# Performance work log

Hardware: AMD Instinct MI355X
Metric: run time of the kernel (lower is better)

## Reference

```python
import jax, jax.numpy as jnp
import numpy as np

B, C, T_TEXT, T_FEAT = 16, 256, 512, 4096
DELTA = 0.1  # temperature


def setup_inputs() -> dict:
    key = jax.random.key(0)
    k1, k2 = jax.random.split(key)
    x = jax.random.normal(k1, (B, C, T_TEXT), dtype=jnp.float32)
    # durations: avg ~8 frames per token so cumsum spans ~T_FEAT frames
    w = jax.random.uniform(k2, (B, T_TEXT), dtype=jnp.float32) * 16.0
    x_mask = jnp.ones((B, T_FEAT), dtype=bool)   # frame-level mask (B, T_feat)
    y_mask = jnp.ones((B, T_TEXT), dtype=bool)   # token-level mask (B, T_text)
    return {"x": x, "w": w, "x_mask": x_mask, "y_mask": y_mask}


def reference(x, w, x_mask, y_mask):
    # x: (B, C, T_text), w: (B, T_text)
    t_feat = x_mask.shape[-1]
    # frame time grid, masked frames zeroed as in reference impl
    t = jnp.arange(t_feat, dtype=x.dtype)[None, :] * x_mask.astype(x.dtype)  # (B, T_feat)
    # Gaussian centers per token: cumulative duration minus half of own duration
    c = jnp.cumsum(w, axis=-1) - 0.5 * w  # (B, T_text)
    # energy: -delta * (t - c)^2  -> (B, T_feat, T_text)
    energy = -DELTA * jnp.square(t[:, :, None] - c[:, None, :])
    energy = jnp.where(y_mask[:, None, :], energy, -jnp.inf)
    attn = jax.nn.softmax(energy, axis=-1)  # softmax over tokens (T_text)
    # weighted sum over tokens: (B, T_feat, T_text) x (B, C, T_text) -> (B, C, T_feat)
    return jnp.einsum('bft,bct->bcf', attn, x)
```

## Files before the change

### kernel.cpp

```cpp
#include <hip/hip_runtime.h>
#include <math.h>


constexpr int BB  = 16;
constexpr int CC  = 256;
constexpr int TT  = 512;
constexpr int TF  = 4096;
constexpr float DEL = 0.1f;

constexpr int TILE_F = 32;
constexpr int MAXW   = 32;
constexpr int MAXN   = 64;
constexpr float CUT  = 200.0f;

__global__ __launch_bounds__(64)
void centers_k(const float* __restrict__ w, float* __restrict__ cw) {
  const int b = blockIdx.x, l = threadIdx.x;
  const float* wr = w + b * TT + l * 8;
  float v[8];
  *(float4*)&v[0] = *(const float4*)&wr[0];
  *(float4*)&v[4] = *(const float4*)&wr[4];
  double s[8]; double run = 0.0;
#pragma unroll
  for (int k = 0; k < 8; ++k) { run += (double)v[k]; s[k] = run; }
  double tot = run;
  for (int off = 1; off < 64; off <<= 1) {
    double o = __shfl_up(tot, off, 64);
    if (l >= off) tot += o;
  }
  const double base = tot - run;
  float* co = cw + b * TT + l * 8;
#pragma unroll
  for (int k = 0; k < 8; ++k) co[k] = (float)(base + s[k] - 0.5 * (double)v[k]);
}

__global__ __launch_bounds__(256, 4)
void gauss_up(const float* __restrict__ x, const float* __restrict__ cw,
              float* __restrict__ out) {
  __shared__ float sc[TT];
  __shared__ __align__(16) float pbuf[MAXN][TILE_F];
  __shared__ int s_info[2];

  const int lin   = blockIdx.x;
  const int xcd   = lin & 7;
  const int slot  = lin >> 3;
  const int b     = xcd * 2 + (slot >> 7);
  const int ftile = slot & 127;
  const int f0    = ftile * TILE_F;
  const int tid   = threadIdx.x;

  sc[tid]       = cw[b * TT + tid];
  sc[tid + 256] = cw[b * TT + tid + 256];
#pragma unroll
  for (int k = 0; k < MAXN * TILE_F / 256; ++k)
    ((float*)pbuf)[tid + 256 * k] = 0.f;
  __syncthreads();

  if (tid < TILE_F) {
    const float fv = (float)(f0 + tid);
    int l = 0, h = TT;
    while (l < h) { int m = (l + h) >> 1; if (sc[m] < fv) l = m + 1; else h = m; }
    int jstar = (l < TT) ? l : TT - 1;
    float dmin = fabsf(sc[jstar] - fv);
    if (l > 0) { float d = fabsf(sc[l - 1] - fv); if (d <= dmin) { dmin = d; jstar = l - 1; } }
    const float D = sqrtf(fmaf(dmin, dmin, CUT));
    int lo = 0; h = TT;
    { const float lv = fv - D;
      while (lo < h) { int m = (lo + h) >> 1; if (sc[m] < lv) lo = m + 1; else h = m; } }
    int hi = lo; h = TT;
    { const float hv = fv + D;
      while (hi < h) { int m = (hi + h) >> 1; if (sc[m] <= hv) hi = m + 1; else h = m; } }
    if (hi - lo > MAXW) {
      int nl = jstar - MAXW / 2; if (nl < lo) nl = lo;
      lo = nl;
      if (hi > lo + MAXW) hi = lo + MAXW;
    }

    int LO = lo, HI = hi;
#pragma unroll
    for (int m = 16; m >= 1; m >>= 1) {
      LO = min(LO, __shfl_xor(LO, m, 32));
      HI = max(HI, __shfl_xor(HI, m, 32));
    }
    int LO4 = LO & ~3;
    if (HI - LO4 > MAXN) {
      const int js0  = __shfl(jstar, 0, 32);
      const int js31 = __shfl(jstar, 31, 32);
      int nl = (((js0 + js31) >> 1) - MAXN / 2) & ~3;
      if (nl < LO4) nl = LO4;
      LO4 = nl;
      if (HI > LO4 + MAXN) HI = LO4 + MAXN;
      if (lo < LO4) lo = LO4;
      if (hi > HI)  hi = HI;
      if (lo >= hi) {
        lo = min(max(jstar, LO4), HI - 1); hi = lo + 1;
      }
    }

    const int n_f = hi - lo;
    const int j0  = lo - LO4;
    const float m0 = DEL * dmin * dmin;
    float Z = 0.f;
    for (int j = 0; j < n_f; ++j) {
      const float d = fv - sc[lo + j];
      const float e = __expf(fmaf(-DEL, d * d, m0));
      pbuf[j0 + j][tid] = e;
      Z += e;
    }
    const float rz = 1.f / Z;
    for (int j = 0; j < n_f; ++j) pbuf[j0 + j][tid] *= rz;
    if (tid == 0) { s_info[0] = LO4; s_info[1] = (HI - LO4 + 3) >> 2; }
  }
  __syncthreads();

  const int LO4 = s_info[0];
  const int NC  = s_info[1];
  const int cg  = tid >> 2;
  const int fg  = tid & 3;

  const float* xr0 = x + ((size_t)b * CC + (size_t)cg * 4) * TT + LO4;

  float acc[4][8];
#pragma unroll
  for (int i = 0; i < 4; ++i)
#pragma unroll
    for (int k = 0; k < 8; ++k) acc[i][k] = 0.f;

  for (int jc = 0; jc < NC; ++jc) {
    float4 xv[4];
#pragma unroll
    for (int i = 0; i < 4; ++i)
      xv[i] = *(const float4*)(xr0 + (size_t)i * TT + 4 * jc);
#pragma unroll
    for (int jj = 0; jj < 4; ++jj) {
      const float4 p0 = *(const float4*)&pbuf[4 * jc + jj][fg * 8];
      const float4 p1 = *(const float4*)&pbuf[4 * jc + jj][fg * 8 + 4];
#pragma unroll
      for (int i = 0; i < 4; ++i) {
        const float xs = ((const float*)&xv[i])[jj];
        acc[i][0] = fmaf(p0.x, xs, acc[i][0]);
        acc[i][1] = fmaf(p0.y, xs, acc[i][1]);
        acc[i][2] = fmaf(p0.z, xs, acc[i][2]);
        acc[i][3] = fmaf(p0.w, xs, acc[i][3]);
        acc[i][4] = fmaf(p1.x, xs, acc[i][4]);
        acc[i][5] = fmaf(p1.y, xs, acc[i][5]);
        acc[i][6] = fmaf(p1.z, xs, acc[i][6]);
        acc[i][7] = fmaf(p1.w, xs, acc[i][7]);
      }
    }
  }

  float* orow = out + ((size_t)b * CC + (size_t)cg * 4) * TF + f0 + fg * 8;
#pragma unroll
  for (int i = 0; i < 4; ++i) {
    *(float4*)(orow + (size_t)i * TF)     =
        make_float4(acc[i][0], acc[i][1], acc[i][2], acc[i][3]);
    *(float4*)(orow + (size_t)i * TF + 4) =
        make_float4(acc[i][4], acc[i][5], acc[i][6], acc[i][7]);
  }
}

extern "C" void kernel_launch(void* const* d_in, const int* in_sizes, int n_in,
                              void* d_out, int out_size, void* d_ws, size_t ws_size,
                              hipStream_t stream) {
  const float* x = (const float*)d_in[0];
  const float* w = (const float*)d_in[1];
  float* out = (float*)d_out;
  float* cw  = (float*)d_ws;

  centers_k<<<dim3(BB), dim3(64), 0, stream>>>(w, cw);
  gauss_up<<<dim3(TF / TILE_F * BB), dim3(256), 0, stream>>>(x, cw, out);
}
```

Baseline: 96.13 us.

## Precompute attention windows in separate kernel and stream weights through workspace

Splits the work differently: a new per-tile kernel recomputes the cumsum centers, does the binary-search window and softmax weights, and writes the weight tile plus window info to workspace. The main kernel then only loads the precomputed weights and does the FMA accumulation, with nontemporal output stores. The goal is to take the serial 32-thread search/softmax phase, which idles most of the block, off the main kernel's critical path. The cost is about 8MB of extra workspace traffic and redundant cumsum work in every tile. A fallback path runs when the workspace is too small.

```diff
diff --git a/kernel.cpp b/kernel.cpp
--- a/kernel.cpp
+++ b/kernel.cpp
@@ -12,6 +12,175 @@
 constexpr int MAXW   = 32;
 constexpr int MAXN   = 64;
 constexpr float CUT  = 200.0f;
+
+constexpr int NTILE = TF / TILE_F * BB;
+constexpr int PBSZ  = MAXN * TILE_F;
+constexpr size_t WS_NEED = 16384 + (size_t)NTILE * PBSZ * 4;
+
+typedef float f32x4 __attribute__((ext_vector_type(4)));
+
+__device__ __forceinline__ void tile_map(int lin, int& b, int& f0) {
+  const int xcd  = lin & 7;
+  const int slot = lin >> 3;
+  b  = xcd * 2 + (slot >> 7);
+  f0 = (slot & 127) * TILE_F;
+}
+
+__global__ __launch_bounds__(64)
+void wins_k(const float* __restrict__ w, float* __restrict__ pb,
+            int2* __restrict__ info) {
+  __shared__ float sc[TT];
+  __shared__ __align__(16) float pbuf[MAXN][TILE_F];
+
+  int b, f0; tile_map(blockIdx.x, b, f0);
+  const int l = threadIdx.x;
+
+  const float* wr = w + b * TT + l * 8;
+  float v[8];
+  *(float4*)&v[0] = *(const float4*)&wr[0];
+  *(float4*)&v[4] = *(const float4*)&wr[4];
+  double s[8]; double run = 0.0;
+#pragma unroll
+  for (int k = 0; k < 8; ++k) { run += (double)v[k]; s[k] = run; }
+  double tot = run;
+  for (int off = 1; off < 64; off <<= 1) {
+    double o = __shfl_up(tot, off, 64);
+    if (l >= off) tot += o;
+  }
+  const double base = tot - run;
+#pragma unroll
+  for (int k = 0; k < 8; ++k)
+    sc[l * 8 + k] = (float)(base + s[k] - 0.5 * (double)v[k]);
+
+#pragma unroll
+  for (int k = 0; k < 8; ++k)
+    ((float4*)pbuf)[l + 64 * k] = make_float4(0.f, 0.f, 0.f, 0.f);
+  __syncthreads();
+
+  if (l < TILE_F) {
+    const float fv = (float)(f0 + l);
+    int lb = 0, h = TT;
+    while (lb < h) { int m = (lb + h) >> 1; if (sc[m] < fv) lb = m + 1; else h = m; }
+    int jstar = (lb < TT) ? lb : TT - 1;
+    float dmin = fabsf(sc[jstar] - fv);
+    if (lb > 0) { float d = fabsf(sc[lb - 1] - fv); if (d <= dmin) { dmin = d; jstar = lb - 1; } }
+    const float D = sqrtf(fmaf(dmin, dmin, CUT));
+    int lo = 0; h = TT;
+    { const float lv = fv - D;
+      while (lo < h) { int m = (lo + h) >> 1; if (sc[m] < lv) lo = m + 1; else h = m; } }
+    int hi = lo; h = TT;
+    { const float hv = fv + D;
+      while (hi < h) { int m = (hi + h) >> 1; if (sc[m] <= hv) hi = m + 1; else h = m; } }
+    if (hi - lo > MAXW) {
+      int nl = jstar - MAXW / 2; if (nl < lo) nl = lo;
+      lo = nl;
+      if (hi > lo + MAXW) hi = lo + MAXW;
+    }
+
+    int LO = lo, HI = hi;
+#pragma unroll
+    for (int m = 16; m >= 1; m >>= 1) {
+      LO = min(LO, __shfl_xor(LO, m, 32));
+      HI = max(HI, __shfl_xor(HI, m, 32));
+    }
+    int LO4 = LO & ~3;
+    if (HI - LO4 > MAXN) {
+      const int js0  = __shfl(jstar, 0, 32);
+      const int js31 = __shfl(jstar, 31, 32);
+      int nl = (((js0 + js31) >> 1) - MAXN / 2) & ~3;
+      if (nl < LO4) nl = LO4;
+      LO4 = nl;
+      if (HI > LO4 + MAXN) HI = LO4 + MAXN;
+      if (lo < LO4) lo = LO4;
+      if (hi > HI)  hi = HI;
+      if (lo >= hi) {
+        lo = min(max(jstar, LO4), HI - 1); hi = lo + 1;
+      }
+    }
+
+    const int n_f = hi - lo;
+    const int j0  = lo - LO4;
+    const float m0 = DEL * dmin * dmin;
+    float Z = 0.f;
+    for (int j = 0; j < n_f; ++j) {
+      const float d = fv - sc[lo + j];
+      const float e = __expf(fmaf(-DEL, d * d, m0));
+      pbuf[j0 + j][l] = e;
+      Z += e;
+    }
+    const float rz = 1.f / Z;
+    for (int j = 0; j < n_f; ++j) pbuf[j0 + j][l] *= rz;
+    if (l == 0) info[blockIdx.x] = make_int2(LO4, (HI - LO4 + 3) >> 2);
+  }
+  __syncthreads();
+
+  float4* dst = (float4*)(pb + (size_t)blockIdx.x * PBSZ);
+#pragma unroll
+  for (int k = 0; k < 8; ++k)
+    dst[l + 64 * k] = ((const float4*)pbuf)[l + 64 * k];
+}
+
+__global__ __launch_bounds__(256, 4)
+void gup2(const float* __restrict__ x, const float* __restrict__ pb,
+          const int2* __restrict__ info, float* __restrict__ out) {
+  __shared__ __align__(16) float pbuf[MAXN][TILE_F];
+
+  int b, f0; tile_map(blockIdx.x, b, f0);
+  const int tid = threadIdx.x;
+  const int2 nfo = info[blockIdx.x];
+
+  const float4* src = (const float4*)(pb + (size_t)blockIdx.x * PBSZ);
+  ((float4*)pbuf)[tid]       = src[tid];
+  ((float4*)pbuf)[tid + 256] = src[tid + 256];
+  __syncthreads();
+
+  const int LO4 = nfo.x;
+  const int NC  = nfo.y;
+  const int cg  = tid >> 2;
+  const int fg  = tid & 3;
+
+  const float* xr0 = x + ((size_t)b * CC + (size_t)cg * 4) * TT + LO4;
+
+  float acc[4][8];
+#pragma unroll
+  for (int i = 0; i < 4; ++i)
+#pragma unroll
+    for (int k = 0; k < 8; ++k) acc[i][k] = 0.f;
+
+  for (int jc = 0; jc < NC; ++jc) {
+    float4 xv[4];
+#pragma unroll
+    for (int i = 0; i < 4; ++i)
+      xv[i] = *(const float4*)(xr0 + (size_t)i * TT + 4 * jc);
+#pragma unroll
+    for (int jj = 0; jj < 4; ++jj) {
+      const float4 p0 = *(const float4*)&pbuf[4 * jc + jj][fg * 8];
+      const float4 p1 = *(const float4*)&pbuf[4 * jc + jj][fg * 8 + 4];
+#pragma unroll
+      for (int i = 0; i < 4; ++i) {
+        const float xs = ((const float*)&xv[i])[jj];
+        acc[i][0] = fmaf(p0.x, xs, acc[i][0]);
+        acc[i][1] = fmaf(p0.y, xs, acc[i][1]);
+        acc[i][2] = fmaf(p0.z, xs, acc[i][2]);
+        acc[i][3] = fmaf(p0.w, xs, acc[i][3]);
+        acc[i][4] = fmaf(p1.x, xs, acc[i][4]);
+        acc[i][5] = fmaf(p1.y, xs, acc[i][5]);
+        acc[i][6] = fmaf(p1.z, xs, acc[i][6]);
+        acc[i][7] = fmaf(p1.w, xs, acc[i][7]);
+      }
+    }
+  }
+
+  float* orow = out + ((size_t)b * CC + (size_t)cg * 4) * TF + f0 + fg * 8;
+#pragma unroll
+  for (int i = 0; i < 4; ++i) {
+    f32x4 v0 = {acc[i][0], acc[i][1], acc[i][2], acc[i][3]};
+    f32x4 v1 = {acc[i][4], acc[i][5], acc[i][6], acc[i][7]};
+    __builtin_nontemporal_store(v0, (f32x4*)(orow + (size_t)i * TF));
+    __builtin_nontemporal_store(v1, (f32x4*)(orow + (size_t)i * TF + 4));
+  }
+}
+
 
 __global__ __launch_bounds__(64)
 void centers_k(const float* __restrict__ w, float* __restrict__ cw) {
@@ -166,8 +335,15 @@
   const float* x = (const float*)d_in[0];
   const float* w = (const float*)d_in[1];
   float* out = (float*)d_out;
-  float* cw  = (float*)d_ws;
-
-  centers_k<<<dim3(BB), dim3(64), 0, stream>>>(w, cw);
-  gauss_up<<<dim3(TF / TILE_F * BB), dim3(256), 0, stream>>>(x, cw, out);
-}
+
+  if (ws_size >= WS_NEED) {
+    int2*  info = (int2*)d_ws;
+    float* pb   = (float*)d_ws + 4096;
+    wins_k<<<dim3(NTILE), dim3(64),  0, stream>>>(w, pb, info);
+    gup2  <<<dim3(NTILE), dim3(256), 0, stream>>>(x, pb, info, out);
+  } else {
+    float* cw = (float*)d_ws;
+    centers_k<<<dim3(BB),    dim3(64),  0, stream>>>(w, cw);
+    gauss_up <<<dim3(NTILE), dim3(256), 0, stream>>>(x, cw, out);
+  }
+}
```

Result: slower. 115.8 us (+20.5%).

## Precompute per-frame token windows in prep kernel and defer softmax normalization

Applied to the files above, without the earlier changes.

The per-frame binary searches for the Gaussian window move out of the main kernel into a wider prep kernel, which writes (argmin, lo, hi) per frame to workspace. The main kernel no longer stages centers or zeroes pbuf in shared memory. It computes exponentials over the whole tile window with vectorized center loads and masking, and applies 1/Z at output time. The thread mapping changes to 8 channels by 4 frames per thread. Using the union window per frame instead of each frame's own window changes numerics slightly and adds a workspace round trip.

```diff
diff --git a/kernel.cpp b/kernel.cpp
--- a/kernel.cpp
+++ b/kernel.cpp
@@ -13,70 +13,90 @@
 constexpr int MAXN   = 64;
 constexpr float CUT  = 200.0f;
 
-__global__ __launch_bounds__(64)
-void centers_k(const float* __restrict__ w, float* __restrict__ cw) {
-  const int b = blockIdx.x, l = threadIdx.x;
-  const float* wr = w + b * TT + l * 8;
-  float v[8];
-  *(float4*)&v[0] = *(const float4*)&wr[0];
-  *(float4*)&v[4] = *(const float4*)&wr[4];
-  double s[8]; double run = 0.0;
+constexpr int NTILE = TF / TILE_F * BB;
+constexpr size_t WS_CW  = (size_t)BB * TT * 4;
+constexpr size_t WS_NEED = WS_CW + (size_t)BB * TF * 8;
+
+__device__ __forceinline__ void tile_map(int lin, int& b, int& f0) {
+  const int xcd  = lin & 7;
+  const int slot = lin >> 3;
+  b  = xcd * 2 + (slot >> 7);
+  f0 = (slot & 127) * TILE_F;
+}
+
+__global__ __launch_bounds__(256)
+void prep_k(const float* __restrict__ w, float* __restrict__ cw,
+            ushort4* __restrict__ win) {
+  __shared__ float sc[TT];
+  const int b = blockIdx.x, tid = threadIdx.x;
+
+  if (tid < 64) {
+    const int l = tid;
+    const float* wr = w + b * TT + l * 8;
+    float v[8];
+    *(float4*)&v[0] = *(const float4*)&wr[0];
+    *(float4*)&v[4] = *(const float4*)&wr[4];
+    double s[8]; double run = 0.0;
 #pragma unroll
-  for (int k = 0; k < 8; ++k) { run += (double)v[k]; s[k] = run; }
-  double tot = run;
-  for (int off = 1; off < 64; off <<= 1) {
-    double o = __shfl_up(tot, off, 64);
-    if (l >= off) tot += o;
+    for (int k = 0; k < 8; ++k) { run += (double)v[k]; s[k] = run; }
+    double tot = run;
+    for (int off = 1; off < 64; off <<= 1) {
+      double o = __shfl_up(tot, off, 64);
+      if (l >= off) tot += o;
+    }
+    const double base = tot - run;
+    float c8[8];
+#pragma unroll
+    for (int k = 0; k < 8; ++k) c8[k] = (float)(base + s[k] - 0.5 * (double)v[k]);
+#pragma unroll
+    for (int k = 0; k < 8; ++k) sc[l * 8 + k] = c8[k];
+    if (blockIdx.y == 0) {
+      float* co = cw + b * TT + l * 8;
+#pragma unroll
+      for (int k = 0; k < 8; ++k) co[k] = c8[k];
+    }
   }
-  const double base = tot - run;
-  float* co = cw + b * TT + l * 8;
-#pragma unroll
-  for (int k = 0; k < 8; ++k) co[k] = (float)(base + s[k] - 0.5 * (double)v[k]);
+  __syncthreads();
+
+  const int f = blockIdx.y * 256 + tid;
+  const float fv = (float)f;
+  int lb = 0, h = TT;
+  while (lb < h) { int m = (lb + h) >> 1; if (sc[m] < fv) lb = m + 1; else h = m; }
+  int js = (lb < TT) ? lb : TT - 1;
+  float dmin = fabsf(sc[js] - fv);
+  if (lb > 0) { float d = fabsf(sc[lb - 1] - fv); if (d <= dmin) { dmin = d; js = lb - 1; } }
+  const float D = sqrtf(fmaf(dmin, dmin, CUT));
+  int lo = 0; h = TT;
+  { const float lv = fv - D;
+    while (lo < h) { int m = (lo + h) >> 1; if (sc[m] < lv) lo = m + 1; else h = m; } }
+  int hi = lo; h = TT;
+  { const float hv = fv + D;
+    while (hi < h) { int m = (hi + h) >> 1; if (sc[m] <= hv) hi = m + 1; else h = m; } }
+  if (hi - lo > MAXW) {
+    int nl = js - MAXW / 2; if (nl < lo) nl = lo;
+    lo = nl;
+    if (hi > lo + MAXW) hi = lo + MAXW;
+  }
+  win[b * TF + f] = make_ushort4((unsigned short)js, (unsigned short)lo,
+                                 (unsigned short)hi, 0);
 }
 
 __global__ __launch_bounds__(256, 4)
 void gauss_up(const float* __restrict__ x, const float* __restrict__ cw,
-              float* __restrict__ out) {
-  __shared__ float sc[TT];
+              const ushort4* __restrict__ win, float* __restrict__ out) {
   __shared__ __align__(16) float pbuf[MAXN][TILE_F];
+  __shared__ float srz[TILE_F];
   __shared__ int s_info[2];
 
-  const int lin   = blockIdx.x;
-  const int xcd   = lin & 7;
-  const int slot  = lin >> 3;
-  const int b     = xcd * 2 + (slot >> 7);
-  const int ftile = slot & 127;
-  const int f0    = ftile * TILE_F;
-  const int tid   = threadIdx.x;
-
-  sc[tid]       = cw[b * TT + tid];
-  sc[tid + 256] = cw[b * TT + tid + 256];
-#pragma unroll
-  for (int k = 0; k < MAXN * TILE_F / 256; ++k)
-    ((float*)pbuf)[tid + 256 * k] = 0.f;
-  __syncthreads();
+  int b, f0; tile_map(blockIdx.x, b, f0);
+  const int tid = threadIdx.x;
+  const float* cwb = cw + b * TT;
 
   if (tid < TILE_F) {
+    const ushort4 wv = win[b * TF + f0 + tid];
+    const int js = wv.x;
+    int LO = wv.y, HI = wv.z;
     const float fv = (float)(f0 + tid);
-    int l = 0, h = TT;
-    while (l < h) { int m = (l + h) >> 1; if (sc[m] < fv) l = m + 1; else h = m; }
-    int jstar = (l < TT) ? l : TT - 1;
-    float dmin = fabsf(sc[jstar] - fv);
-    if (l > 0) { float d = fabsf(sc[l - 1] - fv); if (d <= dmin) { dmin = d; jstar = l - 1; } }
-    const float D = sqrtf(fmaf(dmin, dmin, CUT));
-    int lo = 0; h = TT;
-    { const float lv = fv - D;
-      while (lo < h) { int m = (lo + h) >> 1; if (sc[m] < lv) lo = m + 1; else h = m; } }
-    int hi = lo; h = TT;
-    { const float hv = fv + D;
-      while (hi < h) { int m = (hi + h) >> 1; if (sc[m] <= hv) hi = m + 1; else h = m; } }
-    if (hi - lo > MAXW) {
-      int nl = jstar - MAXW / 2; if (nl < lo) nl = lo;
-      lo = nl;
-      if (hi > lo + MAXW) hi = lo + MAXW;
-    }
-
-    int LO = lo, HI = hi;
 #pragma unroll
     for (int m = 16; m >= 1; m >>= 1) {
       LO = min(LO, __shfl_xor(LO, m, 32));
@@ -84,79 +104,80 @@
     }
     int LO4 = LO & ~3;
     if (HI - LO4 > MAXN) {
-      const int js0  = __shfl(jstar, 0, 32);
-      const int js31 = __shfl(jstar, 31, 32);
+      const int js0  = __shfl(js, 0, 32);
+      const int js31 = __shfl(js, 31, 32);
       int nl = (((js0 + js31) >> 1) - MAXN / 2) & ~3;
       if (nl < LO4) nl = LO4;
       LO4 = nl;
       if (HI > LO4 + MAXN) HI = LO4 + MAXN;
-      if (lo < LO4) lo = LO4;
-      if (hi > HI)  hi = HI;
-      if (lo >= hi) {
-        lo = min(max(jstar, LO4), HI - 1); hi = lo + 1;
-      }
     }
-
-    const int n_f = hi - lo;
-    const int j0  = lo - LO4;
+    const int n  = HI - LO4;
+    const int NC = (n + 3) >> 2;
+    const float dmin = fabsf(fv - cwb[js]);
     const float m0 = DEL * dmin * dmin;
     float Z = 0.f;
-    for (int j = 0; j < n_f; ++j) {
-      const float d = fv - sc[lo + j];
-      const float e = __expf(fmaf(-DEL, d * d, m0));
-      pbuf[j0 + j][tid] = e;
-      Z += e;
+    for (int jc = 0; jc < NC; ++jc) {
+      const float4 c4 = *(const float4*)(cwb + LO4 + 4 * jc);
+      const int jb = 4 * jc;
+      float d0 = fv - c4.x, d1 = fv - c4.y, d2 = fv - c4.z, d3 = fv - c4.w;
+      float e0 = __expf(fmaf(-DEL, d0 * d0, m0));
+      float e1 = __expf(fmaf(-DEL, d1 * d1, m0));
+      float e2 = __expf(fmaf(-DEL, d2 * d2, m0));
+      float e3 = __expf(fmaf(-DEL, d3 * d3, m0));
+      e0 = (jb + 0 < n) ? e0 : 0.f;
+      e1 = (jb + 1 < n) ? e1 : 0.f;
+      e2 = (jb + 2 < n) ? e2 : 0.f;
+      e3 = (jb + 3 < n) ? e3 : 0.f;
+      pbuf[jb + 0][tid] = e0;
+      pbuf[jb + 1][tid] = e1;
+      pbuf[jb + 2][tid] = e2;
+      pbuf[jb + 3][tid] = e3;
+      Z += (e0 + e1) + (e2 + e3);
     }
-    const float rz = 1.f / Z;
-    for (int j = 0; j < n_f; ++j) pbuf[j0 + j][tid] *= rz;
-    if (tid == 0) { s_info[0] = LO4; s_info[1] = (HI - LO4 + 3) >> 2; }
+    srz[tid] = 1.f / fmaxf(Z, 1e-30f);
+    if (tid == 0) { s_info[0] = LO4; s_info[1] = NC; }
   }
   __syncthreads();
 
   const int LO4 = s_info[0];
   const int NC  = s_info[1];
-  const int cg  = tid >> 2;
-  const int fg  = tid & 3;
+  const int cg  = tid >> 3;
+  const int fg  = tid & 7;
 
-  const float* xr0 = x + ((size_t)b * CC + (size_t)cg * 4) * TT + LO4;
+  const float* xr0 = x + ((size_t)b * CC + (size_t)cg * 8) * TT + LO4;
 
-  float acc[4][8];
+  float acc[8][4];
 #pragma unroll
-  for (int i = 0; i < 4; ++i)
+  for (int i = 0; i < 8; ++i)
 #pragma unroll
-    for (int k = 0; k < 8; ++k) acc[i][k] = 0.f;
+    for (int k = 0; k < 4; ++k) acc[i][k] = 0.f;
 
   for (int jc = 0; jc < NC; ++jc) {
-    float4 xv[4];
+    float4 xv[8];
 #pragma unroll
-    for (int i = 0; i < 4; ++i)
+    for (int i = 0; i < 8; ++i)
       xv[i] = *(const float4*)(xr0 + (size_t)i * TT + 4 * jc);
 #pragma unroll
     for (int jj = 0; jj < 4; ++jj) {
-      const float4 p0 = *(const float4*)&pbuf[4 * jc + jj][fg * 8];
-      const float4 p1 = *(const float4*)&pbuf[4 * jc + jj][fg * 8 + 4];
+      const float4 p = *(const float4*)&pbuf[4 * jc + jj][fg * 4];
 #pragma unroll
-      for (int i = 0; i < 4; ++i) {
+      for (int i = 0; i < 8; ++i) {
         const float xs = ((const float*)&xv[i])[jj];
-        acc[i][0] = fmaf(p0.x, xs, acc[i][0]);
-        acc[i][1] = fmaf(p0.y, xs, acc[i][1]);
-        acc[i][2] = fmaf(p0.z, xs, acc[i][2]);
-        acc[i][3] = fmaf(p0.w, xs, acc[i][3]);
-        acc[i][4] = fmaf(p1.x, xs, acc[i][4]);
-        acc[i][5] = fmaf(p1.y, xs, acc[i][5]);
-        acc[i][6] = fmaf(p1.z, xs, acc[i][6]);
-        acc[i][7] = fmaf(p1.w, xs, acc[i][7]);
+        acc[i][0] = fmaf(p.x, xs, acc[i][0]);
+        acc[i][1] = fmaf(p.y, xs, acc[i][1]);
+        acc[i][2] = fmaf(p.z, xs, acc[i][2]);
+        acc[i][3] = fmaf(p.w, xs, acc[i][3]);
       }
     }
   }
 
-  float* orow = out + ((size_t)b * CC + (size_t)cg * 4) * TF + f0 + fg * 8;
+  const float4 rzv = *(const float4*)&srz[fg * 4];
+  float* orow = out + ((size_t)b * CC + (size_t)cg * 8) * TF + f0 + fg * 4;
 #pragma unroll
-  for (int i = 0; i < 4; ++i) {
-    *(float4*)(orow + (size_t)i * TF)     =
-        make_float4(acc[i][0], acc[i][1], acc[i][2], acc[i][3]);
-    *(float4*)(orow + (size_t)i * TF + 4) =
-        make_float4(acc[i][4], acc[i][5], acc[i][6], acc[i][7]);
+  for (int i = 0; i < 8; ++i) {
+    *(float4*)(orow + (size_t)i * TF) =
+        make_float4(acc[i][0] * rzv.x, acc[i][1] * rzv.y,
+                    acc[i][2] * rzv.z, acc[i][3] * rzv.w);
   }
 }
 
@@ -166,8 +187,10 @@
   const float* x = (const float*)d_in[0];
   const float* w = (const float*)d_in[1];
   float* out = (float*)d_out;
-  float* cw  = (float*)d_ws;
 
-  centers_k<<<dim3(BB), dim3(64), 0, stream>>>(w, cw);
-  gauss_up<<<dim3(TF / TILE_F * BB), dim3(256), 0, stream>>>(x, cw, out);
+  float*   cw  = (float*)d_ws;
+  ushort4* wn  = (ushort4*)((char*)d_ws + WS_CW);
+
+  prep_k  <<<dim3(BB, TF / 256), dim3(256), 0, stream>>>(w, cw, wn);
+  gauss_up<<<dim3(NTILE),        dim3(256), 0, stream>>>(x, cw, wn, out);
 }
```

Result: faster. 94.23 us (-2.0%).
